# Optimization experiments

Measured on AMD Instinct MI355X. Metric: run time of the kernel, lower is better.

## Reference

```python
import jax, jax.numpy as jnp
import numpy as np
import math

N, E = 50000, 800000
HID, EDIM, H = 128, 32, 8
D = HID // H            # head_dim = 16
FFN = 4 * HID           # ModelConstants.FFN_EXPANSION_FACTOR = 4
EPS = 1e-5


def layer_norm(x, g, b):
    mu = jnp.mean(x, axis=-1, keepdims=True)
    var = jnp.var(x, axis=-1, keepdims=True)
    return (x - mu) * jax.lax.rsqrt(var + EPS) * g + b


def setup_inputs() -> dict:
    key = jax.random.key(0)
    ks = jax.random.split(key, 16)
    s = 1.0 / math.sqrt(HID)
    inp = {
        "x": jax.random.normal(ks[0], (N, HID), jnp.float32),
        "edge_index": jax.random.randint(ks[1], (2, E), 0, N, jnp.int32),
        "edge_attr": jax.random.normal(ks[2], (E, EDIM), jnp.float32),
        # projections stored as (in, out): y = x @ W + b (same math as torch Linear)
        "qW": jax.random.normal(ks[3], (HID, HID), jnp.float32) * s,
        "qb": jnp.zeros((HID,), jnp.float32),
        "kW": jax.random.normal(ks[4], (HID, HID), jnp.float32) * s,
        "kb": jnp.zeros((HID,), jnp.float32),
        "vW": jax.random.normal(ks[5], (HID, HID), jnp.float32) * s,
        "vb": jnp.zeros((HID,), jnp.float32),
        "eW": jax.random.normal(ks[6], (EDIM, H), jnp.float32) / math.sqrt(EDIM),
        "eb": jnp.zeros((H,), jnp.float32),
        "oW": jax.random.normal(ks[7], (HID, HID), jnp.float32) * s,
        "ob": jnp.zeros((HID,), jnp.float32),
        "ln1_g": jnp.ones((HID,), jnp.float32),
        "ln1_b": jnp.zeros((HID,), jnp.float32),
        "f1W": jax.random.normal(ks[8], (HID, FFN), jnp.float32) * s,
        "f1b": jnp.zeros((FFN,), jnp.float32),
        "lnf_g": jnp.ones((FFN,), jnp.float32),
        "lnf_b": jnp.zeros((FFN,), jnp.float32),
        "f2W": jax.random.normal(ks[9], (FFN, HID), jnp.float32) / math.sqrt(FFN),
        "f2b": jnp.zeros((HID,), jnp.float32),
        "ln2_g": jnp.ones((HID,), jnp.float32),
        "ln2_b": jnp.zeros((HID,), jnp.float32),
    }
    return inp


def reference(x, edge_index, edge_attr, qW, qb, kW, kb, vW, vb, eW, eb, oW, ob,
              ln1_g, ln1_b, f1W, f1b, lnf_g, lnf_b, f2W, f2b, ln2_g, ln2_b):
    src, dst = edge_index[0], edge_index[1]
    q = (x @ qW + qb).reshape(N, H, D)
    k = (x @ kW + kb).reshape(N, H, D)
    v = (x @ vW + vb).reshape(N, H, D)
    edge_bias = edge_attr @ eW + eb                     # (E, H)
    # per-edge attention scores
    scores = jnp.sum(q[src] * k[dst], axis=-1) / math.sqrt(D) + edge_bias  # (E, H)
    # scatter softmax over edges grouped by dst
    mx = jax.ops.segment_max(scores, dst, num_segments=N)  # (N, H), -inf for empty
    mx = jnp.where(jnp.isinf(mx), jnp.zeros_like(mx), mx)
    ex = jnp.exp(scores - mx[dst])                      # (E, H)
    den = jax.ops.segment_sum(ex, dst, num_segments=N)
    den = jnp.maximum(den, 1e-8)
    attn = ex / den[dst]                                # (E, H)
    # weighted aggregation
    wv = v[src] * attn[:, :, None]                      # (E, H, D)
    out = jax.ops.segment_sum(wv, dst, num_segments=N)  # (N, H, D)
    out = out.reshape(N, HID) @ oW + ob
    x = layer_norm(x + out, ln1_g, ln1_b)
    h = x @ f1W + f1b
    h = jax.nn.gelu(layer_norm(h, lnf_g, lnf_b), approximate=False)
    h = h @ f2W + f2b
    x = layer_norm(x + h, ln2_g, ln2_b)
    return x
```

## Files before the change

### kernel.cpp

```cpp
#include <hip/hip_runtime.h>
#include <math.h>

#define LN_EPS 1e-5f

typedef __attribute__((ext_vector_type(8))) __bf16 bf16x8;
typedef __attribute__((ext_vector_type(4))) float f32x4;

__device__ inline float bf2f(unsigned short u) {
  union { unsigned int i; float f; } x; x.i = ((unsigned int)u) << 16; return x.f;
}
__device__ inline unsigned short f2bf(float f) {
  union { float f; unsigned int i; } x; x.f = f;
  unsigned int r = (x.i + 0x7FFFu + ((x.i >> 16) & 1u)) >> 16;
  return (unsigned short)r;
}
__device__ inline void gload_lds16(const void* g, void* l) {
  __builtin_amdgcn_global_load_lds((const __attribute__((address_space(1))) void*)g,
                                   (__attribute__((address_space(3))) void*)l, 16, 0, 0);
}

__global__ __launch_bounds__(256)
void to_bf16(const float* __restrict__ in, unsigned short* __restrict__ outp, long n) {
  long i = ((long)blockIdx.x * 256 + threadIdx.x) * 4;
  if (i >= n) return;
  float4 v = *(const float4*)&in[i];
  ushort4 o = { f2bf(v.x), f2bf(v.y), f2bf(v.z), f2bf(v.w) };
  *(ushort4*)&outp[i] = o;
}

__global__ __launch_bounds__(256)
void prep_weights(const float* qW, const float* kW, const float* vW, const float* oW,
                  const float* f1W, const float* f2W,
                  unsigned short* qkvWt, unsigned short* oWt,
                  unsigned short* f1Wt, unsigned short* f2Wt,
                  const float* qb, const float* kb, const float* vb, float* qkvbias) {
  const int t = blockIdx.x;
  if (t == 192) {
    int i = threadIdx.x;
    if (i < 128) { qkvbias[i] = qb[i]; qkvbias[128 + i] = kb[i]; }
    else if (i < 256) qkvbias[256 + (i - 128)] = vb[i - 128];
    return;
  }
  const float* W; unsigned short* Wt; int K, M, lt;
  if (t < 64)       { K = 128; M = 128; lt = t & 15;
    if (t < 16)      { W = qW; Wt = qkvWt; }
    else if (t < 32) { W = kW; Wt = qkvWt + 16384; }
    else if (t < 48) { W = vW; Wt = qkvWt + 32768; }
    else             { W = oW; Wt = oWt; } }
  else if (t < 128) { K = 128; M = 512; lt = t - 64; W = f1W; Wt = f1Wt; }
  else              { K = 512; M = 128; lt = t - 128; W = f2W; Wt = f2Wt; }
  const int ktiles = K >> 5;
  const int k0 = (lt % ktiles) * 32, m0 = (lt / ktiles) * 32;
  __shared__ float tb[32][33];
  const int tx = threadIdx.x & 31, ty = threadIdx.x >> 5;
#pragma unroll
  for (int i = 0; i < 32; i += 8)
    tb[ty + i][tx] = W[(size_t)(k0 + ty + i) * M + m0 + tx];
  __syncthreads();
#pragma unroll
  for (int i = 0; i < 32; i += 8)
    Wt[(size_t)(m0 + ty + i) * K + k0 + tx] = f2bf(tb[tx][ty + i]);
}

template<bool OBF>
__global__ __launch_bounds__(256)
void gemm_mfma(const unsigned short* __restrict__ A, const unsigned short* __restrict__ Wt,
               const float* __restrict__ bias, void* __restrict__ Cout,
               int Nr, int K, int M) {
  __shared__ __align__(16) unsigned short As[128 * 64];
  __shared__ __align__(16) unsigned short Bs[128 * 64];
  const int tid = threadIdx.x;
  const int bm = blockIdx.x * 128, bn = blockIdx.y * 128;
  const int lane = tid & 63;
  const int wr = (tid >> 6) >> 1, wc = (tid >> 6) & 1;
  f32x4 acc[4][4] = {};
  const int nkt = K >> 6;
  for (int kt = 0; kt < nkt; ++kt) {
#pragma unroll
    for (int i = 0; i < 4; ++i) {
      int c = tid + i * 256;
      int row = c >> 3;
      int j = (c & 7) ^ (row & 7);
      int ar = bm + row; ar = ar < Nr ? ar : Nr - 1;
      gload_lds16(A + (size_t)ar * K + kt * 64 + j * 8, As + (size_t)c * 8);
      gload_lds16(Wt + (size_t)(bn + row) * K + kt * 64 + j * 8, Bs + (size_t)c * 8);
    }
    __syncthreads();
#pragma unroll
    for (int ks = 0; ks < 2; ++ks) {
      bf16x8 af[4], bfr[4];
#pragma unroll
      for (int f = 0; f < 4; ++f) {
        int rowa = wr * 64 + f * 16 + (lane & 15);
        int ja = (ks * 4 + (lane >> 4)) ^ (rowa & 7);
        af[f] = *(const bf16x8*)(As + rowa * 64 + ja * 8);
        int rowb = wc * 64 + f * 16 + (lane & 15);
        int jb = (ks * 4 + (lane >> 4)) ^ (rowb & 7);
        bfr[f] = *(const bf16x8*)(Bs + rowb * 64 + jb * 8);
      }
#pragma unroll
      for (int fr = 0; fr < 4; ++fr)
#pragma unroll
        for (int fc = 0; fc < 4; ++fc)
          acc[fr][fc] = __builtin_amdgcn_mfma_f32_16x16x32_bf16(af[fr], bfr[fc], acc[fr][fc], 0, 0, 0);
    }
    __syncthreads();
  }
#pragma unroll
  for (int fr = 0; fr < 4; ++fr) {
#pragma unroll
    for (int j = 0; j < 4; ++j) {
      int row = bm + wr * 64 + fr * 16 + (lane >> 4) * 4 + j;
      if (row < Nr) {
#pragma unroll
        for (int fc = 0; fc < 4; ++fc) {
          int col = bn + wc * 64 + fc * 16 + (lane & 15);
          float v = acc[fr][fc][j] + bias[col];
          if (OBF) ((unsigned short*)Cout)[(size_t)row * M + col] = f2bf(v);
          else     ((float*)Cout)[(size_t)row * M + col] = v;
        }
      }
    }
  }
}

template<bool WF32, bool WBF, bool RESBF>
__global__ __launch_bounds__(256)
void gemm_ln(const unsigned short* __restrict__ A, const unsigned short* __restrict__ Wt,
             const float* __restrict__ bias, const void* __restrict__ res,
             const float* __restrict__ g, const float* __restrict__ b,
             float* __restrict__ y, unsigned short* __restrict__ ybf, int Nr, int K) {
  __shared__ __align__(16) unsigned short As[128 * 64];
  __shared__ __align__(16) unsigned short Bs[128 * 64];
  __shared__ float pls[128][2], plss[128][2];
  const int tid = threadIdx.x;
  const int bm = blockIdx.x * 128;
  const int lane = tid & 63;
  const int wr = (tid >> 6) >> 1, wc = (tid >> 6) & 1;
  f32x4 acc[4][4] = {};
  const int nkt = K >> 6;
  for (int kt = 0; kt < nkt; ++kt) {
#pragma unroll
    for (int i = 0; i < 4; ++i) {
      int c = tid + i * 256;
      int row = c >> 3;
      int j = (c & 7) ^ (row & 7);
      int ar = bm + row; ar = ar < Nr ? ar : Nr - 1;
      gload_lds16(A + (size_t)ar * K + kt * 64 + j * 8, As + (size_t)c * 8);
      gload_lds16(Wt + (size_t)row * K + kt * 64 + j * 8, Bs + (size_t)c * 8);
    }
    __syncthreads();
#pragma unroll
    for (int ks = 0; ks < 2; ++ks) {
      bf16x8 af[4], bfr[4];
#pragma unroll
      for (int f = 0; f < 4; ++f) {
        int rowa = wr * 64 + f * 16 + (lane & 15);
        int ja = (ks * 4 + (lane >> 4)) ^ (rowa & 7);
        af[f] = *(const bf16x8*)(As + rowa * 64 + ja * 8);
        int rowb = wc * 64 + f * 16 + (lane & 15);
        int jb = (ks * 4 + (lane >> 4)) ^ (rowb & 7);
        bfr[f] = *(const bf16x8*)(Bs + rowb * 64 + jb * 8);
      }
#pragma unroll
      for (int fr = 0; fr < 4; ++fr)
#pragma unroll
        for (int fc = 0; fc < 4; ++fc)
          acc[fr][fc] = __builtin_amdgcn_mfma_f32_16x16x32_bf16(af[fr], bfr[fc], acc[fr][fc], 0, 0, 0);
    }
    __syncthreads();
  }
#pragma unroll
  for (int fr = 0; fr < 4; ++fr) {
#pragma unroll
    for (int j = 0; j < 4; ++j) {
      const int rl = wr * 64 + fr * 16 + (lane >> 4) * 4 + j;
      const int row = bm + rl;
      const int rowc = row < Nr ? row : Nr - 1;
      float s = 0.f, ss = 0.f;
#pragma unroll
      for (int fc = 0; fc < 4; ++fc) {
        int col = wc * 64 + fc * 16 + (lane & 15);
        float rv = RESBF ? bf2f(((const unsigned short*)res)[(size_t)rowc * 128 + col])
                         : ((const float*)res)[(size_t)rowc * 128 + col];
        float val = acc[fr][fc][j] + bias[col] + rv;
        acc[fr][fc][j] = val;
        s += val; ss += val * val;
      }
      s += __shfl_xor(s, 1); ss += __shfl_xor(ss, 1);
      s += __shfl_xor(s, 2); ss += __shfl_xor(ss, 2);
      s += __shfl_xor(s, 4); ss += __shfl_xor(ss, 4);
      s += __shfl_xor(s, 8); ss += __shfl_xor(ss, 8);
      if ((lane & 15) == 0) { pls[rl][wc] = s; plss[rl][wc] = ss; }
    }
  }
  __syncthreads();
#pragma unroll
  for (int fr = 0; fr < 4; ++fr) {
#pragma unroll
    for (int j = 0; j < 4; ++j) {
      const int rl = wr * 64 + fr * 16 + (lane >> 4) * 4 + j;
      const int row = bm + rl;
      if (row >= Nr) continue;
      const float S = pls[rl][0] + pls[rl][1];
      const float SS = plss[rl][0] + plss[rl][1];
      const float mu = S * (1.f / 128.f);
      const float inv = rsqrtf(SS * (1.f / 128.f) - mu * mu + LN_EPS);
#pragma unroll
      for (int fc = 0; fc < 4; ++fc) {
        int col = wc * 64 + fc * 16 + (lane & 15);
        float o = (acc[fr][fc][j] - mu) * inv * g[col] + b[col];
        if (WF32) y[(size_t)row * 128 + col] = o;
        if (WBF)  ybf[(size_t)row * 128 + col] = f2bf(o);
      }
    }
  }
}

__global__ __launch_bounds__(256)
void edge_hist_bias(const int* __restrict__ ei, const float* __restrict__ ea,
                    const float* __restrict__ eW, const float* __restrict__ eb,
                    int* __restrict__ deg, unsigned short* __restrict__ ebias_seq, int E) {
  __shared__ float ews[256];
  __shared__ float ebs[8];
  const int tid = threadIdx.x;
  if (tid < 256) ews[tid] = eW[tid];
  if (tid < 8) ebs[tid] = eb[tid];
  __syncthreads();
  int e = blockIdx.x * 256 + tid;
  if (e >= E) return;
  atomicAdd(&deg[ei[E + e]], 1);
  float bias[8];
#pragma unroll
  for (int h = 0; h < 8; ++h) bias[h] = ebs[h];
#pragma unroll
  for (int i4 = 0; i4 < 8; ++i4) {
    float4 a = *(const float4*)&ea[(size_t)e * 32 + i4 * 4];
    float av[4] = {a.x, a.y, a.z, a.w};
#pragma unroll
    for (int j = 0; j < 4; ++j)
#pragma unroll
      for (int h = 0; h < 8; ++h) bias[h] += av[j] * ews[(i4 * 4 + j) * 8 + h];
  }
  union { unsigned short us[8]; uint4 v; } pk;
#pragma unroll
  for (int h = 0; h < 8; ++h) pk.us[h] = f2bf(bias[h]);
  *(uint4*)&ebias_seq[(size_t)e * 8] = pk.v;
}

__global__ __launch_bounds__(256)
void deg_block_sum(const int* __restrict__ deg, int* __restrict__ bsum, int N) {
  const int t = threadIdx.x;
  const int beg = blockIdx.x * 2048 + t * 8;
  int s = 0;
#pragma unroll
  for (int j = 0; j < 8; ++j) { int i = beg + j; if (i < N) s += deg[i]; }
#pragma unroll
  for (int off = 32; off; off >>= 1) s += __shfl_xor(s, off);
  __shared__ int ws[4];
  if ((t & 63) == 0) ws[t >> 6] = s;
  __syncthreads();
  if (t == 0) bsum[blockIdx.x] = ws[0] + ws[1] + ws[2] + ws[3];
}

__global__ __launch_bounds__(64)
void scan_bsum(int* __restrict__ bsum, int* __restrict__ offs_last, int nb) {
  const int t = threadIdx.x;
  int v = (t < nb) ? bsum[t] : 0;
  int inc = v;
#pragma unroll
  for (int off = 1; off < 64; off <<= 1) {
    int x = __shfl_up(inc, off);
    if (t >= off) inc += x;
  }
  if (t < nb) bsum[t] = inc - v;
  if (t == 63) *offs_last = inc;
}

__global__ __launch_bounds__(256)
void deg_scan_write(const int* __restrict__ deg, const int* __restrict__ bsum,
                    int* __restrict__ offs, int* __restrict__ pos, int N) {
  const int t = threadIdx.x;
  const int beg = blockIdx.x * 2048 + t * 8;
  int loc[8]; int T = 0;
#pragma unroll
  for (int j = 0; j < 8; ++j) { int i = beg + j; loc[j] = (i < N) ? deg[i] : 0; T += loc[j]; }
  int inc = T;
#pragma unroll
  for (int off = 1; off < 64; off <<= 1) {
    int x = __shfl_up(inc, off);
    if ((t & 63) >= off) inc += x;
  }
  __shared__ int ws[4];
  if ((t & 63) == 63) ws[t >> 6] = inc;
  __syncthreads();
  const int wid = t >> 6;
  int wbase = 0;
  for (int w = 0; w < wid; ++w) wbase += ws[w];
  int base = bsum[blockIdx.x] + wbase + inc - T;
#pragma unroll
  for (int j = 0; j < 8; ++j) {
    int i = beg + j;
    if (i < N) { offs[i] = base; pos[i] = base; base += loc[j]; }
  }
}

__global__ __launch_bounds__(256)
void edge_scatter_pb(const int* __restrict__ ei, int* __restrict__ pos,
                     const unsigned short* __restrict__ ebias_seq,
                     int* __restrict__ csr_src, unsigned short* __restrict__ ebp, int E) {
  int e = blockIdx.x * 256 + threadIdx.x;
  if (e >= E) return;
  int d = ei[E + e];
  uint4 pk = *(const uint4*)&ebias_seq[(size_t)e * 8];
  int p = atomicAdd(&pos[d], 1);
  csr_src[p] = ei[e];
  *(uint4*)&ebp[(size_t)p * 8] = pk;
}

__global__ __launch_bounds__(256)
void node_agg(const int* __restrict__ csr_src, const int* __restrict__ offs,
              const unsigned short* __restrict__ qkv, const unsigned short* __restrict__ ebp,
              unsigned short* __restrict__ agg, int N) {
  const int wid = threadIdx.x >> 6, lane = threadIdx.x & 63;
  const int h = lane >> 3;
  const long n = (long)blockIdx.x * 4 + wid;
  if (n >= N) return;
  const int off = offs[n], end = offs[n + 1];
  const ushort2 kv2 = *(const ushort2*)&qkv[(size_t)n * 384 + 128 + lane * 2];
  const float k0 = bf2f(kv2.x), k1 = bf2f(kv2.y);
  float acc0 = 0.f, acc1 = 0.f, den = 0.f;
  int i = off;
  for (; i + 8 <= end; i += 8) {
    size_t bb[8];
#pragma unroll
    for (int u = 0; u < 8; ++u) bb[u] = (size_t)csr_src[i + u] * 384;
    ushort2 qv[8], vv[8];
#pragma unroll
    for (int u = 0; u < 8; ++u) qv[u] = *(const ushort2*)&qkv[bb[u] + lane * 2];
#pragma unroll
    for (int u = 0; u < 8; ++u) vv[u] = *(const ushort2*)&qkv[bb[u] + 256 + lane * 2];
    float ebv[8];
#pragma unroll
    for (int u = 0; u < 8; ++u) ebv[u] = bf2f(ebp[(size_t)(i + u) * 8 + h]);
    float p[8];
#pragma unroll
    for (int u = 0; u < 8; ++u) p[u] = bf2f(qv[u].x) * k0 + bf2f(qv[u].y) * k1;
#pragma unroll
    for (int u = 0; u < 8; ++u) {
      p[u] += __shfl_xor(p[u], 1);
      p[u] += __shfl_xor(p[u], 2);
      p[u] += __shfl_xor(p[u], 4);
    }
#pragma unroll
    for (int u = 0; u < 8; ++u) {
      const float ex = __expf(p[u] * 0.25f + ebv[u]);
      den += ex;
      acc0 += bf2f(vv[u].x) * ex;
      acc1 += bf2f(vv[u].y) * ex;
    }
  }
  for (; i + 4 <= end; i += 4) {
    size_t bb[4];
#pragma unroll
    for (int u = 0; u < 4; ++u) bb[u] = (size_t)csr_src[i + u] * 384;
    ushort2 qv[4], vv[4];
#pragma unroll
    for (int u = 0; u < 4; ++u) qv[u] = *(const ushort2*)&qkv[bb[u] + lane * 2];
#pragma unroll
    for (int u = 0; u < 4; ++u) vv[u] = *(const ushort2*)&qkv[bb[u] + 256 + lane * 2];
    float ebv[4];
#pragma unroll
    for (int u = 0; u < 4; ++u) ebv[u] = bf2f(ebp[(size_t)(i + u) * 8 + h]);
    float p[4];
#pragma unroll
    for (int u = 0; u < 4; ++u) p[u] = bf2f(qv[u].x) * k0 + bf2f(qv[u].y) * k1;
#pragma unroll
    for (int u = 0; u < 4; ++u) {
      p[u] += __shfl_xor(p[u], 1);
      p[u] += __shfl_xor(p[u], 2);
      p[u] += __shfl_xor(p[u], 4);
    }
#pragma unroll
    for (int u = 0; u < 4; ++u) {
      const float ex = __expf(p[u] * 0.25f + ebv[u]);
      den += ex;
      acc0 += bf2f(vv[u].x) * ex;
      acc1 += bf2f(vv[u].y) * ex;
    }
  }
  for (; i < end; ++i) {
    const size_t b0 = (size_t)csr_src[i] * 384;
    const ushort2 qa = *(const ushort2*)&qkv[b0 + lane * 2];
    const ushort2 va = *(const ushort2*)&qkv[b0 + 256 + lane * 2];
    float p = bf2f(qa.x) * k0 + bf2f(qa.y) * k1;
    p += __shfl_xor(p, 1);
    p += __shfl_xor(p, 2);
    p += __shfl_xor(p, 4);
    const float ex = __expf(p * 0.25f + bf2f(ebp[(size_t)i * 8 + h]));
    den += ex;
    acc0 += bf2f(va.x) * ex;
    acc1 += bf2f(va.y) * ex;
  }
  const float r = 1.f / fmaxf(den, 1e-8f);
  ushort2 o; o.x = f2bf(acc0 * r); o.y = f2bf(acc1 * r);
  *(ushort2*)&agg[(size_t)n * 128 + lane * 2] = o;
}

__global__ __launch_bounds__(256)
void ln_gelu512(unsigned short* __restrict__ hbuf, const float* __restrict__ g,
                const float* __restrict__ b, int Nr) {
  __shared__ float rs[4], rss[4];
  const long row = blockIdx.x;
  const int tid = threadIdx.x;
  ushort2 u = *(ushort2*)&hbuf[row * 512 + tid * 2];
  float v0 = bf2f(u.x), v1 = bf2f(u.y);
  float s = v0 + v1, ss = v0 * v0 + v1 * v1;
#pragma unroll
  for (int off = 32; off; off >>= 1) { s += __shfl_xor(s, off); ss += __shfl_xor(ss, off); }
  const int wid = tid >> 6, lane = tid & 63;
  if (lane == 0) { rs[wid] = s; rss[wid] = ss; }
  __syncthreads();
  s = rs[0] + rs[1] + rs[2] + rs[3];
  ss = rss[0] + rss[1] + rss[2] + rss[3];
  const float mu = s * (1.f / 512.f);
  const float inv = rsqrtf(ss * (1.f / 512.f) - mu * mu + LN_EPS);
  float t0 = (v0 - mu) * inv * g[tid * 2] + b[tid * 2];
  float t1 = (v1 - mu) * inv * g[tid * 2 + 1] + b[tid * 2 + 1];
  t0 = 0.5f * t0 * (1.f + erff(t0 * 0.70710678118654752f));
  t1 = 0.5f * t1 * (1.f + erff(t1 * 0.70710678118654752f));
  ushort2 o; o.x = f2bf(t0); o.y = f2bf(t1);
  *(ushort2*)&hbuf[row * 512 + tid * 2] = o;
}

extern "C" void kernel_launch(void* const* d_in, const int* in_sizes, int n_in,
                              void* d_out, int out_size, void* d_ws, size_t ws_size,
                              hipStream_t stream) {
  const float* x   = (const float*)d_in[0];
  const int*   ei  = (const int*)d_in[1];
  const float* ea  = (const float*)d_in[2];
  const float* qW  = (const float*)d_in[3];
  const float* qbi = (const float*)d_in[4];
  const float* kW  = (const float*)d_in[5];
  const float* kbi = (const float*)d_in[6];
  const float* vW  = (const float*)d_in[7];
  const float* vbi = (const float*)d_in[8];
  const float* eW  = (const float*)d_in[9];
  const float* eb  = (const float*)d_in[10];
  const float* oW  = (const float*)d_in[11];
  const float* ob  = (const float*)d_in[12];
  const float* ln1_g = (const float*)d_in[13];
  const float* ln1_b = (const float*)d_in[14];
  const float* f1W = (const float*)d_in[15];
  const float* f1b = (const float*)d_in[16];
  const float* lnf_g = (const float*)d_in[17];
  const float* lnf_b = (const float*)d_in[18];
  const float* f2W = (const float*)d_in[19];
  const float* f2b = (const float*)d_in[20];
  const float* ln2_g = (const float*)d_in[21];
  const float* ln2_b = (const float*)d_in[22];
  float* out = (float*)d_out;

  const int N = in_sizes[0] / 128;
  const int E = in_sizes[1] / 2;
  const size_t NH = (size_t)N * 128;

  float* F = (float*)d_ws;
  unsigned short* xbf   = (unsigned short*)F;
  unsigned short* qkvb  = (unsigned short*)(F + NH / 2);
  unsigned short* ebp   = (unsigned short*)(F + 2 * NH);
  unsigned short* aggb  = (unsigned short*)(F + 2 * NH + NH / 2);
  unsigned short* ebias_seq = (unsigned short*)(F + 3 * NH);
  unsigned short* x1bf  = xbf;
  unsigned short* hbufb = (unsigned short*)(F + NH / 2);
  int* ib      = (int*)(F + 4 * NH);
  int* csr_src = ib;
  int* offs    = ib + E;
  int* pos     = ib + E + N + 1;
  int* bsum    = ib + E + 2 * N + 1;
  unsigned short* wt = (unsigned short*)(ib + E + 2 * N + 128);
  unsigned short* qkvWt = wt;
  unsigned short* oWt   = wt + 49152;
  unsigned short* f1Wt  = wt + 65536;
  unsigned short* f2Wt  = wt + 131072;
  float* qkvbias = (float*)(wt + 196608);

  dim3 blk(256);
  dim3 gqkv((N + 127) / 128, 3);
  dim3 g128((N + 127) / 128, 1);
  dim3 gf1((N + 127) / 128, 4);
  const int nb = (N + 2047) / 2048;
  const int ge = (E + 255) / 256;

  to_bf16<<<dim3((int)((NH / 4 + 255) / 256)), blk, 0, stream>>>(x, xbf, (long)NH);
  prep_weights<<<dim3(193), blk, 0, stream>>>(qW, kW, vW, oW, f1W, f2W,
                                              qkvWt, oWt, f1Wt, f2Wt,
                                              qbi, kbi, vbi, qkvbias);

  gemm_mfma<true><<<gqkv, blk, 0, stream>>>(xbf, qkvWt, qkvbias, qkvb, N, 128, 384);

  hipMemsetAsync(pos, 0, (size_t)N * sizeof(int), stream);
  edge_hist_bias<<<dim3(ge), blk, 0, stream>>>(ei, ea, eW, eb, pos, ebias_seq, E);
  deg_block_sum<<<dim3(nb), blk, 0, stream>>>(pos, bsum, N);
  scan_bsum<<<dim3(1), dim3(64), 0, stream>>>(bsum, offs + N, nb);
  deg_scan_write<<<dim3(nb), blk, 0, stream>>>(pos, bsum, offs, pos, N);
  edge_scatter_pb<<<dim3(ge), blk, 0, stream>>>(ei, pos, ebias_seq, csr_src, ebp, E);

  node_agg<<<dim3((N + 3) / 4), blk, 0, stream>>>(csr_src, offs, qkvb, ebp, aggb, N);

  gemm_ln<false, true, true><<<g128, blk, 0, stream>>>(aggb, oWt, ob, xbf,
                                                       ln1_g, ln1_b, nullptr, x1bf, N, 128);

  gemm_mfma<true><<<gf1, blk, 0, stream>>>(x1bf, f1Wt, f1b, hbufb, N, 128, 512);
  ln_gelu512<<<dim3(N), blk, 0, stream>>>(hbufb, lnf_g, lnf_b, N);
  gemm_ln<true, false, true><<<g128, blk, 0, stream>>>(hbufb, f2Wt, f2b, x1bf,
                                                       ln2_g, ln2_b, out, nullptr, N, 512);
}
```

Baseline: 318.6 us.

## Replace degree-scan CSR build with two-level bucketed binning by destination

After: 507.0 us. +59.1%, slower.

```diff
diff --git a/kernel.cpp b/kernel.cpp
--- a/kernel.cpp
+++ b/kernel.cpp
@@ -2,6 +2,7 @@
 #include <math.h>
 
 #define LN_EPS 1e-5f
+#define CAPB 2816
 
 typedef __attribute__((ext_vector_type(8))) __bf16 bf16x8;
 typedef __attribute__((ext_vector_type(4))) float f32x4;
@@ -20,23 +21,31 @@
 }
 
 __global__ __launch_bounds__(256)
-void to_bf16(const float* __restrict__ in, unsigned short* __restrict__ outp, long n) {
-  long i = ((long)blockIdx.x * 256 + threadIdx.x) * 4;
-  if (i >= n) return;
-  float4 v = *(const float4*)&in[i];
-  ushort4 o = { f2bf(v.x), f2bf(v.y), f2bf(v.z), f2bf(v.w) };
-  *(ushort4*)&outp[i] = o;
-}
-
-__global__ __launch_bounds__(256)
-void prep_weights(const float* qW, const float* kW, const float* vW, const float* oW,
-                  const float* f1W, const float* f2W,
-                  unsigned short* qkvWt, unsigned short* oWt,
-                  unsigned short* f1Wt, unsigned short* f2Wt,
-                  const float* qb, const float* kb, const float* vb, float* qkvbias) {
-  const int t = blockIdx.x;
+void front(const float* __restrict__ x, unsigned short* __restrict__ xbf, long n,
+           int* __restrict__ bcnt, int nbuck, int* __restrict__ ovf_cnt, int gA,
+           const float* qW, const float* kW, const float* vW, const float* oW,
+           const float* f1W, const float* f2W,
+           unsigned short* qkvWt, unsigned short* oWt,
+           unsigned short* f1Wt, unsigned short* f2Wt,
+           const float* qb, const float* kb, const float* vb, float* qkvbias) {
+  const int b = blockIdx.x;
+  const int tid = threadIdx.x;
+  if (b < gA) {
+    long i = ((long)b * 256 + tid) * 4;
+    if (i >= n) return;
+    float4 v = *(const float4*)&x[i];
+    ushort4 o = { f2bf(v.x), f2bf(v.y), f2bf(v.z), f2bf(v.w) };
+    *(ushort4*)&xbf[i] = o;
+    return;
+  }
+  if (b == gA) {
+    for (int i = tid; i < nbuck; i += 256) bcnt[i] = 0;
+    if (tid == 0) *ovf_cnt = 0;
+    return;
+  }
+  const int t = b - gA - 1;
   if (t == 192) {
-    int i = threadIdx.x;
+    int i = tid;
     if (i < 128) { qkvbias[i] = qb[i]; qkvbias[128 + i] = kb[i]; }
     else if (i < 256) qkvbias[256 + (i - 128)] = vb[i - 128];
     return;
@@ -52,7 +61,7 @@
   const int ktiles = K >> 5;
   const int k0 = (lt % ktiles) * 32, m0 = (lt / ktiles) * 32;
   __shared__ float tb[32][33];
-  const int tx = threadIdx.x & 31, ty = threadIdx.x >> 5;
+  const int tx = tid & 31, ty = tid >> 5;
 #pragma unroll
   for (int i = 0; i < 32; i += 8)
     tb[ty + i][tx] = W[(size_t)(k0 + ty + i) * M + m0 + tx];
@@ -218,9 +227,11 @@
 }
 
 __global__ __launch_bounds__(256)
-void edge_hist_bias(const int* __restrict__ ei, const float* __restrict__ ea,
-                    const float* __restrict__ eW, const float* __restrict__ eb,
-                    int* __restrict__ deg, unsigned short* __restrict__ ebias_seq, int E) {
+void edge_bin(const int* __restrict__ ei, const float* __restrict__ ea,
+              const float* __restrict__ eW, const float* __restrict__ eb,
+              int* __restrict__ bcnt, uint2* __restrict__ sd_arr, uint4* __restrict__ bias_arr,
+              int* __restrict__ ovf_cnt, uint2* __restrict__ ovf_sd, uint4* __restrict__ ovf_bias,
+              int E) {
   __shared__ float ews[256];
   __shared__ float ebs[8];
   const int tid = threadIdx.x;
@@ -229,7 +240,7 @@
   __syncthreads();
   int e = blockIdx.x * 256 + tid;
   if (e >= E) return;
-  atomicAdd(&deg[ei[E + e]], 1);
+  const int src = ei[e], dst = ei[E + e];
   float bias[8];
 #pragma unroll
   for (int h = 0; h < 8; ++h) bias[h] = ebs[h];
@@ -245,77 +256,102 @@
   union { unsigned short us[8]; uint4 v; } pk;
 #pragma unroll
   for (int h = 0; h < 8; ++h) pk.us[h] = f2bf(bias[h]);
-  *(uint4*)&ebias_seq[(size_t)e * 8] = pk.v;
-}
-
-__global__ __launch_bounds__(256)
-void deg_block_sum(const int* __restrict__ deg, int* __restrict__ bsum, int N) {
+  const int b = dst >> 7;
+  const int p = atomicAdd(&bcnt[b], 1);
+  if (p < CAPB) {
+    sd_arr[(size_t)b * CAPB + p] = make_uint2((unsigned)src, (unsigned)dst);
+    bias_arr[(size_t)b * CAPB + p] = pk.v;
+  } else {
+    int o = atomicAdd(ovf_cnt, 1);
+    if (o < 4096) { ovf_sd[o] = make_uint2((unsigned)src, (unsigned)dst); ovf_bias[o] = pk.v; }
+  }
+}
+
+__global__ __launch_bounds__(512)
+void bucket_scan(const int* __restrict__ bcnt, int* __restrict__ bbase,
+                 int* __restrict__ offs_N, int nb, int E) {
+  __shared__ int sm[512];
   const int t = threadIdx.x;
-  const int beg = blockIdx.x * 2048 + t * 8;
-  int s = 0;
-#pragma unroll
-  for (int j = 0; j < 8; ++j) { int i = beg + j; if (i < N) s += deg[i]; }
-#pragma unroll
-  for (int off = 32; off; off >>= 1) s += __shfl_xor(s, off);
-  __shared__ int ws[4];
-  if ((t & 63) == 0) ws[t >> 6] = s;
-  __syncthreads();
-  if (t == 0) bsum[blockIdx.x] = ws[0] + ws[1] + ws[2] + ws[3];
-}
-
-__global__ __launch_bounds__(64)
-void scan_bsum(int* __restrict__ bsum, int* __restrict__ offs_last, int nb) {
-  const int t = threadIdx.x;
-  int v = (t < nb) ? bsum[t] : 0;
-  int inc = v;
-#pragma unroll
-  for (int off = 1; off < 64; off <<= 1) {
-    int x = __shfl_up(inc, off);
-    if (t >= off) inc += x;
-  }
-  if (t < nb) bsum[t] = inc - v;
-  if (t == 63) *offs_last = inc;
-}
-
-__global__ __launch_bounds__(256)
-void deg_scan_write(const int* __restrict__ deg, const int* __restrict__ bsum,
-                    int* __restrict__ offs, int* __restrict__ pos, int N) {
-  const int t = threadIdx.x;
-  const int beg = blockIdx.x * 2048 + t * 8;
-  int loc[8]; int T = 0;
-#pragma unroll
-  for (int j = 0; j < 8; ++j) { int i = beg + j; loc[j] = (i < N) ? deg[i] : 0; T += loc[j]; }
-  int inc = T;
-#pragma unroll
-  for (int off = 1; off < 64; off <<= 1) {
-    int x = __shfl_up(inc, off);
-    if ((t & 63) >= off) inc += x;
-  }
-  __shared__ int ws[4];
-  if ((t & 63) == 63) ws[t >> 6] = inc;
-  __syncthreads();
-  const int wid = t >> 6;
-  int wbase = 0;
-  for (int w = 0; w < wid; ++w) wbase += ws[w];
-  int base = bsum[blockIdx.x] + wbase + inc - T;
-#pragma unroll
-  for (int j = 0; j < 8; ++j) {
-    int i = beg + j;
-    if (i < N) { offs[i] = base; pos[i] = base; base += loc[j]; }
-  }
-}
-
-__global__ __launch_bounds__(256)
-void edge_scatter_pb(const int* __restrict__ ei, int* __restrict__ pos,
-                     const unsigned short* __restrict__ ebias_seq,
-                     int* __restrict__ csr_src, unsigned short* __restrict__ ebp, int E) {
-  int e = blockIdx.x * 256 + threadIdx.x;
-  if (e >= E) return;
-  int d = ei[E + e];
-  uint4 pk = *(const uint4*)&ebias_seq[(size_t)e * 8];
-  int p = atomicAdd(&pos[d], 1);
-  csr_src[p] = ei[e];
-  *(uint4*)&ebp[(size_t)p * 8] = pk;
+  int v = (t < nb) ? bcnt[t] : 0;
+  sm[t] = v;
+  __syncthreads();
+  for (int off = 1; off < 512; off <<= 1) {
+    int x = (t >= off) ? sm[t - off] : 0;
+    __syncthreads();
+    sm[t] += x;
+    __syncthreads();
+  }
+  if (t < nb) bbase[t] = sm[t] - v;
+  if (t == nb - 1) bbase[nb] = sm[t];
+  if (t == 0) *offs_N = E;
+}
+
+__global__ __launch_bounds__(256)
+void bucket_scatter(const uint2* __restrict__ sd_arr, const uint4* __restrict__ bias_arr,
+                    const int* __restrict__ bcnt, const int* __restrict__ bbase,
+                    const int* __restrict__ ovf_cnt, const uint2* __restrict__ ovf_sd,
+                    const uint4* __restrict__ ovf_bias,
+                    int* __restrict__ csr_src, unsigned short* __restrict__ ebp,
+                    int* __restrict__ offs, int N) {
+  const int b = blockIdx.x;
+  const int tid = threadIdx.x;
+  const int dst0 = b << 7;
+  const int ndst = min(128, N - dst0);
+  const int base = bbase[b];
+  const int cnt_true = bcnt[b];
+  const int cnt_in = min(cnt_true, CAPB);
+  __shared__ int lcnt[128], loff[128], wsum2[2];
+  __shared__ int stage_src[CAPB];
+  __shared__ uint4 stage_bias[CAPB];
+  if (tid < 128) lcnt[tid] = 0;
+  __syncthreads();
+  const uint2* sd = sd_arr + (size_t)b * CAPB;
+  const uint4* ba = bias_arr + (size_t)b * CAPB;
+  for (int i = tid; i < cnt_in; i += 256) atomicAdd(&lcnt[(int)sd[i].y - dst0], 1);
+  const int novf = *ovf_cnt;
+  for (int j = tid; j < novf; j += 256) {
+    uint2 s = ovf_sd[j];
+    if ((int)(s.y >> 7) == b) atomicAdd(&lcnt[(int)s.y - dst0], 1);
+  }
+  __syncthreads();
+  {
+    const int lane = tid & 63;
+    int v = (tid < 128) ? lcnt[tid] : 0;
+    int inc = v;
+#pragma unroll
+    for (int off = 1; off < 64; off <<= 1) {
+      int x = __shfl_up(inc, off);
+      if (lane >= off) inc += x;
+    }
+    if (tid < 128 && lane == 63) wsum2[tid >> 6] = inc;
+    __syncthreads();
+    if (tid < 128) loff[tid] = inc - v + ((tid >= 64) ? wsum2[0] : 0);
+  }
+  __syncthreads();
+  if (tid < ndst) offs[dst0 + tid] = base + loff[tid];
+  if (tid < 128) lcnt[tid] = loff[tid];
+  __syncthreads();
+  for (int i = tid; i < cnt_in; i += 256) {
+    uint2 s = sd[i];
+    uint4 bi = ba[i];
+    int p = atomicAdd(&lcnt[(int)s.y - dst0], 1);
+    if (p < CAPB) { stage_src[p] = (int)s.x; stage_bias[p] = bi; }
+    else { csr_src[base + p] = (int)s.x; *(uint4*)&ebp[(size_t)(base + p) * 8] = bi; }
+  }
+  for (int j = tid; j < novf; j += 256) {
+    uint2 s = ovf_sd[j];
+    if ((int)(s.y >> 7) != b) continue;
+    uint4 bi = ovf_bias[j];
+    int p = atomicAdd(&lcnt[(int)s.y - dst0], 1);
+    if (p < CAPB) { stage_src[p] = (int)s.x; stage_bias[p] = bi; }
+    else { csr_src[base + p] = (int)s.x; *(uint4*)&ebp[(size_t)(base + p) * 8] = bi; }
+  }
+  __syncthreads();
+  const int nst = min(cnt_true, CAPB);
+  for (int i = tid; i < nst; i += 256) {
+    csr_src[base + i] = stage_src[i];
+    *(uint4*)&ebp[(size_t)(base + i) * 8] = stage_bias[i];
+  }
 }
 
 __global__ __launch_bounds__(256)
@@ -464,21 +500,26 @@
   const int N = in_sizes[0] / 128;
   const int E = in_sizes[1] / 2;
   const size_t NH = (size_t)N * 128;
+  const int NBUCK = (N + 127) >> 7;
 
   float* F = (float*)d_ws;
   unsigned short* xbf   = (unsigned short*)F;
   unsigned short* qkvb  = (unsigned short*)(F + NH / 2);
   unsigned short* ebp   = (unsigned short*)(F + 2 * NH);
   unsigned short* aggb  = (unsigned short*)(F + 2 * NH + NH / 2);
-  unsigned short* ebias_seq = (unsigned short*)(F + 3 * NH);
   unsigned short* x1bf  = xbf;
   unsigned short* hbufb = (unsigned short*)(F + NH / 2);
-  int* ib      = (int*)(F + 4 * NH);
-  int* csr_src = ib;
-  int* offs    = ib + E;
-  int* pos     = ib + E + N + 1;
-  int* bsum    = ib + E + 2 * N + 1;
-  unsigned short* wt = (unsigned short*)(ib + E + 2 * N + 128);
+  int* ib        = (int*)(F + 3 * NH);
+  uint2* sd_arr  = (uint2*)ib;
+  uint4* bias_arr = (uint4*)(ib + 2 * (size_t)NBUCK * CAPB);
+  int* csr_src   = ib + 6 * (size_t)NBUCK * CAPB;
+  int* offs      = csr_src + E;
+  int* bcnt      = offs + N + 4;
+  int* bbase     = bcnt + ((NBUCK + 3) & ~3);
+  int* ovf_cnt   = bbase + ((NBUCK + 4) & ~3);
+  uint2* ovf_sd  = (uint2*)(ovf_cnt + 4);
+  uint4* ovf_bias = (uint4*)(ovf_cnt + 4 + 8192);
+  unsigned short* wt = (unsigned short*)(ovf_cnt + 4 + 8192 + 16384);
   unsigned short* qkvWt = wt;
   unsigned short* oWt   = wt + 49152;
   unsigned short* f1Wt  = wt + 65536;
@@ -489,22 +530,22 @@
   dim3 gqkv((N + 127) / 128, 3);
   dim3 g128((N + 127) / 128, 1);
   dim3 gf1((N + 127) / 128, 4);
-  const int nb = (N + 2047) / 2048;
   const int ge = (E + 255) / 256;
-
-  to_bf16<<<dim3((int)((NH / 4 + 255) / 256)), blk, 0, stream>>>(x, xbf, (long)NH);
-  prep_weights<<<dim3(193), blk, 0, stream>>>(qW, kW, vW, oW, f1W, f2W,
-                                              qkvWt, oWt, f1Wt, f2Wt,
-                                              qbi, kbi, vbi, qkvbias);
+  const int gA = (int)((NH / 4 + 255) / 256);
+
+  front<<<dim3(gA + 1 + 193), blk, 0, stream>>>(x, xbf, (long)NH, bcnt, NBUCK, ovf_cnt, gA,
+                                                qW, kW, vW, oW, f1W, f2W,
+                                                qkvWt, oWt, f1Wt, f2Wt,
+                                                qbi, kbi, vbi, qkvbias);
 
   gemm_mfma<true><<<gqkv, blk, 0, stream>>>(xbf, qkvWt, qkvbias, qkvb, N, 128, 384);
 
-  hipMemsetAsync(pos, 0, (size_t)N * sizeof(int), stream);
-  edge_hist_bias<<<dim3(ge), blk, 0, stream>>>(ei, ea, eW, eb, pos, ebias_seq, E);
-  deg_block_sum<<<dim3(nb), blk, 0, stream>>>(pos, bsum, N);
-  scan_bsum<<<dim3(1), dim3(64), 0, stream>>>(bsum, offs + N, nb);
-  deg_scan_write<<<dim3(nb), blk, 0, stream>>>(pos, bsum, offs, pos, N);
-  edge_scatter_pb<<<dim3(ge), blk, 0, stream>>>(ei, pos, ebias_seq, csr_src, ebp, E);
+  edge_bin<<<dim3(ge), blk, 0, stream>>>(ei, ea, eW, eb, bcnt, sd_arr, bias_arr,
+                                         ovf_cnt, ovf_sd, ovf_bias, E);
+  bucket_scan<<<dim3(1), dim3(512), 0, stream>>>(bcnt, bbase, offs + N, NBUCK, E);
+  bucket_scatter<<<dim3(NBUCK), blk, 0, stream>>>(sd_arr, bias_arr, bcnt, bbase,
+                                                  ovf_cnt, ovf_sd, ovf_bias,
+                                                  csr_src, ebp, offs, N);
 
   node_agg<<<dim3((N + 3) / 4), blk, 0, stream>>>(csr_src, offs, qkvb, ebp, aggb, N);
 
```

## Fuse front-end prep kernels and partition edge scatter by destination range

Applied to the files above, without the earlier changes.

Measured after the change: 299.8 us. 5.9% less time.

```diff
diff --git a/kernel.cpp b/kernel.cpp
--- a/kernel.cpp
+++ b/kernel.cpp
@@ -20,23 +20,32 @@
 }
 
 __global__ __launch_bounds__(256)
-void to_bf16(const float* __restrict__ in, unsigned short* __restrict__ outp, long n) {
-  long i = ((long)blockIdx.x * 256 + threadIdx.x) * 4;
-  if (i >= n) return;
-  float4 v = *(const float4*)&in[i];
-  ushort4 o = { f2bf(v.x), f2bf(v.y), f2bf(v.z), f2bf(v.w) };
-  *(ushort4*)&outp[i] = o;
-}
-
-__global__ __launch_bounds__(256)
-void prep_weights(const float* qW, const float* kW, const float* vW, const float* oW,
-                  const float* f1W, const float* f2W,
-                  unsigned short* qkvWt, unsigned short* oWt,
-                  unsigned short* f1Wt, unsigned short* f2Wt,
-                  const float* qb, const float* kb, const float* vb, float* qkvbias) {
-  const int t = blockIdx.x;
+void front(const float* __restrict__ x, unsigned short* __restrict__ xbf, long n,
+           int* __restrict__ pos, int N, int gA, int gZ,
+           const float* qW, const float* kW, const float* vW, const float* oW,
+           const float* f1W, const float* f2W,
+           unsigned short* qkvWt, unsigned short* oWt,
+           unsigned short* f1Wt, unsigned short* f2Wt,
+           const float* qb, const float* kb, const float* vb, float* qkvbias) {
+  const int b = blockIdx.x;
+  const int tid = threadIdx.x;
+  if (b < gA) {
+    long i = ((long)b * 256 + tid) * 4;
+    if (i >= n) return;
+    float4 v = *(const float4*)&x[i];
+    ushort4 o = { f2bf(v.x), f2bf(v.y), f2bf(v.z), f2bf(v.w) };
+    *(ushort4*)&xbf[i] = o;
+    return;
+  }
+  if (b < gA + gZ) {
+    int base = (b - gA) * 1024 + tid * 4;
+    if (base + 3 < N) *(int4*)(pos + base) = make_int4(0, 0, 0, 0);
+    else for (int j = 0; j < 4; ++j) if (base + j < N) pos[base + j] = 0;
+    return;
+  }
+  const int t = b - gA - gZ;
   if (t == 192) {
-    int i = threadIdx.x;
+    int i = tid;
     if (i < 128) { qkvbias[i] = qb[i]; qkvbias[128 + i] = kb[i]; }
     else if (i < 256) qkvbias[256 + (i - 128)] = vb[i - 128];
     return;
@@ -52,7 +61,7 @@
   const int ktiles = K >> 5;
   const int k0 = (lt % ktiles) * 32, m0 = (lt / ktiles) * 32;
   __shared__ float tb[32][33];
-  const int tx = threadIdx.x & 31, ty = threadIdx.x >> 5;
+  const int tx = tid & 31, ty = tid >> 5;
 #pragma unroll
   for (int i = 0; i < 32; i += 8)
     tb[ty + i][tx] = W[(size_t)(k0 + ty + i) * M + m0 + tx];
@@ -306,16 +315,28 @@
 }
 
 __global__ __launch_bounds__(256)
-void edge_scatter_pb(const int* __restrict__ ei, int* __restrict__ pos,
-                     const unsigned short* __restrict__ ebias_seq,
-                     int* __restrict__ csr_src, unsigned short* __restrict__ ebp, int E) {
-  int e = blockIdx.x * 256 + threadIdx.x;
-  if (e >= E) return;
-  int d = ei[E + e];
-  uint4 pk = *(const uint4*)&ebias_seq[(size_t)e * 8];
-  int p = atomicAdd(&pos[d], 1);
-  csr_src[p] = ei[e];
-  *(uint4*)&ebp[(size_t)p * 8] = pk;
+void edge_scatter_part(const int* __restrict__ ei, int* __restrict__ pos,
+                       const unsigned short* __restrict__ ebias_seq,
+                       int* __restrict__ csr_src, unsigned short* __restrict__ ebp,
+                       int E, int N) {
+  const int part = blockIdx.x & 7;
+  const int slice = blockIdx.x >> 3;
+  const int nslice = gridDim.x >> 3;
+  const int per = (E + nslice - 1) / nslice;
+  const int lo = slice * per;
+  const int hi = min(E, lo + per);
+  const int drange = (N + 7) >> 3;
+  const int dlo = part * drange;
+  const int dhi = min(N, dlo + drange);
+  for (int e = lo + threadIdx.x; e < hi; e += 256) {
+    int d = ei[E + e];
+    if (d < dlo || d >= dhi) continue;
+    int s = ei[e];
+    uint4 bi = *(const uint4*)&ebias_seq[(size_t)e * 8];
+    int p = atomicAdd(&pos[d], 1);
+    csr_src[p] = s;
+    *(uint4*)&ebp[(size_t)p * 8] = bi;
+  }
 }
 
 __global__ __launch_bounds__(256)
@@ -491,20 +512,21 @@
   dim3 gf1((N + 127) / 128, 4);
   const int nb = (N + 2047) / 2048;
   const int ge = (E + 255) / 256;
-
-  to_bf16<<<dim3((int)((NH / 4 + 255) / 256)), blk, 0, stream>>>(x, xbf, (long)NH);
-  prep_weights<<<dim3(193), blk, 0, stream>>>(qW, kW, vW, oW, f1W, f2W,
-                                              qkvWt, oWt, f1Wt, f2Wt,
-                                              qbi, kbi, vbi, qkvbias);
+  const int gA = (int)((NH / 4 + 255) / 256);
+  const int gZ = (N + 1023) / 1024;
+
+  front<<<dim3(gA + gZ + 193), blk, 0, stream>>>(x, xbf, (long)NH, pos, N, gA, gZ,
+                                                 qW, kW, vW, oW, f1W, f2W,
+                                                 qkvWt, oWt, f1Wt, f2Wt,
+                                                 qbi, kbi, vbi, qkvbias);
 
   gemm_mfma<true><<<gqkv, blk, 0, stream>>>(xbf, qkvWt, qkvbias, qkvb, N, 128, 384);
 
-  hipMemsetAsync(pos, 0, (size_t)N * sizeof(int), stream);
   edge_hist_bias<<<dim3(ge), blk, 0, stream>>>(ei, ea, eW, eb, pos, ebias_seq, E);
   deg_block_sum<<<dim3(nb), blk, 0, stream>>>(pos, bsum, N);
   scan_bsum<<<dim3(1), dim3(64), 0, stream>>>(bsum, offs + N, nb);
   deg_scan_write<<<dim3(nb), blk, 0, stream>>>(pos, bsum, offs, pos, N);
-  edge_scatter_pb<<<dim3(ge), blk, 0, stream>>>(ei, pos, ebias_seq, csr_src, ebp, E);
+  edge_scatter_part<<<dim3(1024), blk, 0, stream>>>(ei, pos, ebias_seq, csr_src, ebp, E, N);
 
   node_agg<<<dim3((N + 3) / 4), blk, 0, stream>>>(csr_src, offs, qkvb, ebp, aggb, N);
 
```
